# Optimization experiments

Measured on AMD Instinct MI355X. Metric: run time of the kernel, lower is better.

The kernel has to match this reference:

```python
import jax, jax.numpy as jnp
import numpy as np

# --- Mamba2Enc config (matches init_kwargs + mamba_ssm Mamba2 defaults) ---
D_IN = 1024
D_MODEL = 512
N_CLASSES = 2
NLAYERS = 2
D_STATE = 64
D_CONV = 4
EXPAND = 2
HEADDIM = 64
D_INNER = EXPAND * D_MODEL            # 1024
NHEADS = D_INNER // HEADDIM           # 16
CONV_DIM = D_INNER + 2 * D_STATE      # 1152 (ngroups=1)
D_IN_PROJ = 2 * D_INNER + 2 * D_STATE + NHEADS  # 2192
EPS = 1e-5


def setup_inputs() -> dict:
    key = jax.random.key(0)
    ks = jax.random.split(key, 10)
    def w(k, shape, sc=0.02):
        return jax.random.normal(k, shape, jnp.float32) * sc
    x = jax.random.normal(ks[0], (4, 4096, D_IN), jnp.float32)
    # fc1
    W1 = w(ks[1], (D_MODEL, D_IN))
    b1 = jnp.zeros((D_MODEL,), jnp.float32)
    # per-layer params stacked on leading NLAYERS axis
    ln_w = jnp.ones((NLAYERS, D_MODEL), jnp.float32)
    ln_b = jnp.zeros((NLAYERS, D_MODEL), jnp.float32)
    W_in = w(ks[2], (NLAYERS, D_IN_PROJ, D_MODEL))
    conv_w = w(ks[3], (NLAYERS, CONV_DIM, D_CONV), 0.1)
    conv_b = jnp.zeros((NLAYERS, CONV_DIM), jnp.float32)
    # dt_bias so that softplus(dt_bias) ~ [0.001, 0.1] (mamba init range)
    dt_bias = jax.random.uniform(ks[4], (NLAYERS, NHEADS), jnp.float32, -6.0, -2.3)
    A_log = jnp.log(jnp.tile(jnp.arange(1, NHEADS + 1, dtype=jnp.float32), (NLAYERS, 1)))
    Dskip = jnp.ones((NLAYERS, NHEADS), jnp.float32)
    norm_w = jnp.ones((NLAYERS, D_INNER), jnp.float32)
    W_out = w(ks[5], (NLAYERS, D_MODEL, D_INNER))
    # classifier
    Wc = w(ks[6], (N_CLASSES, D_MODEL))
    bc = jnp.zeros((N_CLASSES,), jnp.float32)
    return dict(x=x, W1=W1, b1=b1, ln_w=ln_w, ln_b=ln_b, W_in=W_in,
                conv_w=conv_w, conv_b=conv_b, dt_bias=dt_bias, A_log=A_log,
                Dskip=Dskip, norm_w=norm_w, W_out=W_out, Wc=Wc, bc=bc)


def _layernorm(h, w, b):
    mu = jnp.mean(h, axis=-1, keepdims=True)
    var = jnp.mean(jnp.square(h - mu), axis=-1, keepdims=True)
    return (h - mu) * jax.lax.rsqrt(var + EPS) * w + b


def _silu(x):
    return x * jax.nn.sigmoid(x)


def _mamba2(x, W_in, conv_w, conv_b, dt_bias, A_log, Dskip, norm_w, W_out):
    b, l, _ = x.shape
    zxbcdt = jnp.einsum('bld,ed->ble', x, W_in)  # (b, l, D_IN_PROJ)
    z = zxbcdt[..., :D_INNER]
    xBC = zxbcdt[..., D_INNER:D_INNER + CONV_DIM]
    dt = jax.nn.softplus(zxbcdt[..., -NHEADS:] + dt_bias)  # (b, l, h)
    # causal depthwise conv1d (kernel D_CONV) + silu
    xp = jnp.pad(xBC, ((0, 0), (D_CONV - 1, 0), (0, 0)))
    xBC = sum(xp[:, k:k + l, :] * conv_w[:, k] for k in range(D_CONV)) + conv_b
    xBC = _silu(xBC)
    xh = xBC[..., :D_INNER].reshape(b, l, NHEADS, HEADDIM)
    B = xBC[..., D_INNER:D_INNER + D_STATE]   # (b, l, n) ngroups=1
    C = xBC[..., D_INNER + D_STATE:]          # (b, l, n)
    A = -jnp.exp(A_log)                       # (h,)
    dA = jnp.exp(dt * A)                      # (b, l, h)
    dtx = dt[..., None] * xh                  # (b, l, h, p)

    def step(hstate, inp):
        dA_t, dtx_t, B_t, C_t = inp  # (b,h), (b,h,p), (b,n), (b,n)
        hstate = hstate * dA_t[:, :, None, None] + dtx_t[:, :, None, :] * B_t[:, None, :, None]
        y = jnp.einsum('bn,bhnp->bhp', C_t, hstate)
        return hstate, y

    init = jnp.zeros((b, NHEADS, D_STATE, HEADDIM), x.dtype)
    xs = (dA.transpose(1, 0, 2), dtx.transpose(1, 0, 2, 3),
          B.transpose(1, 0, 2), C.transpose(1, 0, 2))
    _, ys = jax.lax.scan(step, init, xs)      # ys: (l, b, h, p)
    y = ys.transpose(1, 0, 2, 3) + Dskip[None, None, :, None] * xh
    y = y.reshape(b, l, D_INNER)
    # RMSNormGated (norm_before_gate=False): rmsnorm(y * silu(z)) * weight
    y = y * _silu(z)
    y = y * jax.lax.rsqrt(jnp.mean(jnp.square(y), axis=-1, keepdims=True) + EPS) * norm_w
    return jnp.einsum('ble,de->bld', y, W_out)


def reference(x, W1, b1, ln_w, ln_b, W_in, conv_w, conv_b, dt_bias, A_log,
              Dskip, norm_w, W_out, Wc, bc):
    # fc1: Linear + GELU (dropout is identity at eval)
    h = jax.nn.gelu(jnp.einsum('bli,di->bld', x, W1) + b1, approximate=False)
    for i in range(NLAYERS):
        h = h + _mamba2(_layernorm(h, ln_w[i], ln_b[i]), W_in[i], conv_w[i],
                        conv_b[i], dt_bias[i], A_log[i], Dskip[i], norm_w[i], W_out[i])
    return jnp.einsum('bld,cd->blc', h, Wc) + bc
```

## Files before the change

kernel.cpp:

```cpp
#include <hip/hip_runtime.h>
#include <hip/hip_bf16.h>
#include <math.h>

#define BATCH 4
#define SEQ 4096
#define ROWS 16384
#define DIN 1024
#define DMODEL 512
#define DINNER 1024
#define DSTATE 64
#define NH 16
#define HD 64
#define CONVDIM 1152
#define DPROJ 2192
#define NPAD 2304
#define QC 64
#define NCH 64
#define LD 72

typedef __attribute__((ext_vector_type(8))) __bf16 bf16x8;
typedef __attribute__((ext_vector_type(4))) __bf16 bf16x4;
typedef __attribute__((ext_vector_type(4))) float f32x4;

__device__ __forceinline__ float siluf(float x){ return x / (1.f + __expf(-x)); }
__device__ __forceinline__ float geluf(float x){ return 0.5f*x*(1.f + erff(x*0.70710678118654752440f)); }

__device__ __forceinline__ bf16x8 scale8(bf16x8 v, float s){
  bf16x8 r;
  #pragma unroll
  for (int e = 0; e < 8; e++) r[e] = (__bf16)((float)v[e]*s);
  return r;
}

__device__ __forceinline__ void gl_lds16(const void* g, void* l){
  __builtin_amdgcn_global_load_lds((const __attribute__((address_space(1))) void*)g,
                                   (__attribute__((address_space(3))) void*)l, 16, 0, 0);
}

__device__ __forceinline__ bf16x8 cvt8(const float* sp){
  const float4* p = (const float4*)sp;
  float4 a = p[0], b = p[1];
  bf16x8 o;
  o[0]=(__bf16)a.x; o[1]=(__bf16)a.y; o[2]=(__bf16)a.z; o[3]=(__bf16)a.w;
  o[4]=(__bf16)b.x; o[5]=(__bf16)b.y; o[6]=(__bf16)b.z; o[7]=(__bf16)b.w;
  return o;
}

__global__ void cast_bf16_kernel(const float* __restrict__ src, __bf16* __restrict__ dst, long n8){
  long i = (long)blockIdx.x*blockDim.x + threadIdx.x;
  long stride = (long)gridDim.x*blockDim.x;
  for (; i < n8; i += stride) *(bf16x8*)(dst + i*8) = cvt8(src + i*8);
}

#define W1G   (DMODEL*DIN/8)
#define WOG   (2*DMODEL*DINNER/8)
#define WIG   (2L*NPAD*(DMODEL/8))
__global__ void prep_weights(const float* __restrict__ W1, const float* __restrict__ W_out,
                             const float* __restrict__ W_in, __bf16* __restrict__ W1b,
                             __bf16* __restrict__ Woutb, __bf16* __restrict__ Winb){
  long total = W1G + WOG + WIG;
  long i = (long)blockIdx.x*blockDim.x + threadIdx.x;
  long stride = (long)gridDim.x*blockDim.x;
  for (; i < total; i += stride){
    if (i < W1G){
      *(bf16x8*)(W1b + i*8) = cvt8(W1 + i*8);
    } else if (i < W1G + WOG){
      long j = i - W1G;
      *(bf16x8*)(Woutb + j*8) = cvt8(W_out + j*8);
    } else {
      long j = i - W1G - WOG;
      int k8 = (int)(j % (DMODEL/8));
      int n  = (int)((j / (DMODEL/8)) % NPAD);
      int l  = (int)(j / ((long)(DMODEL/8)*NPAD));
      bf16x8 o;
      if (n < DPROJ){
        o = cvt8(W_in + ((long)l*DPROJ + n)*DMODEL + k8*8);
      } else {
        #pragma unroll
        for (int e = 0; e < 8; e++) o[e] = (__bf16)0.f;
      }
      *(bf16x8*)(Winb + ((long)l*NPAD + n)*DMODEL + k8*8) = o;
    }
  }
}

template<typename OutT, int EPI, int BM, int BN>
__global__ __launch_bounds__(256) void gemm_bt(const __bf16* __restrict__ A, const __bf16* __restrict__ Bm,
                                               OutT* __restrict__ C, const float* __restrict__ bias,
                                               int K, int Nc, int nbm){
  constexpr int MI = BM/32, NI = BN/32;
  constexpr int CHA = BM/64;
  constexpr int CHT = (BM+BN)/64;
  __shared__ __align__(16) __bf16 As[3][BM*32];
  __shared__ __align__(16) __bf16 Bs[3][BN*32];
  int nwg = gridDim.x;
  int cpx = nwg >> 3;
  int lin = blockIdx.x;
  int swz = (lin & 7)*cpx + (lin >> 3);
  int bm = swz % nbm, bn = swz / nbm;
  int tid = threadIdx.x;
  int lane = tid & 63, wid = tid >> 6;
  int wm = (wid >> 1)*(BM/2), wn = (wid & 1)*(BN/2);
  int lr = lane & 15, kb = lane >> 4;
  f32x4 acc[MI][NI] = {};
  const char* Ab = (const char*)A + (size_t)bm*BM*(size_t)(K*2);
  const char* Bb = (const char*)Bm + (size_t)bn*BN*(size_t)(K*2);
  int nkk = K >> 5;

  auto STAGE = [&](int kk, int buf){
    #pragma unroll
    for (int it = 0; it < CHT; it++){
      int cbase = it*4096 + wid*1024;
      int off = cbase + lane*16;
      int row = off >> 6, cb = off & 63;
      if (it < CHA) gl_lds16(Ab + (size_t)row*(K*2) + kk*64 + cb, (char*)(&As[buf][0]) + cbase);
      else          gl_lds16(Bb + (size_t)(row - BM)*(K*2) + kk*64 + cb, (char*)(&Bs[buf][0]) + (cbase - BM*64));
    }
  };

  STAGE(0, 0);
  if (nkk > 1) STAGE(1, 1);
  for (int kk = 0; kk < nkk; kk++){
    int cur = kk % 3;
    if (kk + 2 < nkk){
      STAGE(kk + 2, (kk + 2) % 3);
      asm volatile("s_waitcnt vmcnt(%0)" :: "n"(2*CHT) : "memory");
    } else if (kk + 1 < nkk){
      asm volatile("s_waitcnt vmcnt(%0)" :: "n"(CHT) : "memory");
    } else {
      asm volatile("s_waitcnt vmcnt(0)" ::: "memory");
    }
    __builtin_amdgcn_sched_barrier(0);
    __builtin_amdgcn_s_barrier();
    __builtin_amdgcn_sched_barrier(0);
    const __bf16* Asb = &As[cur][0];
    const __bf16* Bsb = &Bs[cur][0];
    bf16x8 af[MI], bfr[NI];
    #pragma unroll
    for (int mi = 0; mi < MI; mi++) af[mi] = *(const bf16x8*)(Asb + (wm + mi*16 + lr)*32 + kb*8);
    #pragma unroll
    for (int ni = 0; ni < NI; ni++) bfr[ni] = *(const bf16x8*)(Bsb + (wn + ni*16 + lr)*32 + kb*8);
    #pragma unroll
    for (int mi = 0; mi < MI; mi++)
      #pragma unroll
      for (int ni = 0; ni < NI; ni++)
        acc[mi][ni] = __builtin_amdgcn_mfma_f32_16x16x32_bf16(af[mi], bfr[ni], acc[mi][ni], 0, 0, 0);
    __builtin_amdgcn_s_barrier();
    __builtin_amdgcn_sched_barrier(0);
  }
  #pragma unroll
  for (int mi = 0; mi < MI; mi++){
    #pragma unroll
    for (int ni = 0; ni < NI; ni++){
      int r0 = bm*BM + wm + mi*16 + (lane >> 4)*4;
      int c  = bn*BN + wn + ni*16 + lr;
      if (c < Nc){
        OutT* Cp = C + (size_t)r0*Nc + c;
        #pragma unroll
        for (int j = 0; j < 4; j++){
          float v = acc[mi][ni][j];
          if (EPI == 1){ float u = v + bias[c]; v = geluf(u); }
          if (EPI == 2){ v += (float)Cp[(size_t)j*Nc]; }
          Cp[(size_t)j*Nc] = (OutT)v;
        }
      }
    }
  }
}

__global__ __launch_bounds__(256) void ln_kernel(const __bf16* __restrict__ h, const float* __restrict__ w,
                                                 const float* __restrict__ b, __bf16* __restrict__ out){
  int row = blockIdx.x*4 + (threadIdx.x >> 6);
  int lane = threadIdx.x & 63;
  const __bf16* hr = h + (size_t)row*DMODEL + lane*8;
  bf16x8 a = *(const bf16x8*)hr;
  float v[8];
  #pragma unroll
  for (int i = 0; i < 8; i++) v[i] = (float)a[i];
  float s = 0.f;
  #pragma unroll
  for (int i = 0; i < 8; i++) s += v[i];
  #pragma unroll
  for (int o = 32; o; o >>= 1) s += __shfl_xor(s, o, 64);
  float mu = s*(1.f/512.f);
  float q = 0.f;
  #pragma unroll
  for (int i = 0; i < 8; i++){ float d = v[i]-mu; q += d*d; }
  #pragma unroll
  for (int o = 32; o; o >>= 1) q += __shfl_xor(q, o, 64);
  float rs = rsqrtf(q*(1.f/512.f) + 1e-5f);
  const float* wp = w + lane*8; const float* bp = b + lane*8;
  bf16x8 o8;
  #pragma unroll
  for (int i = 0; i < 8; i++) o8[i] = (__bf16)((v[i]-mu)*rs*wp[i] + bp[i]);
  *(bf16x8*)(out + (size_t)row*DMODEL + lane*8) = o8;
}

__global__ __launch_bounds__(256) void convdt_kernel(const __bf16* __restrict__ zx, const float* __restrict__ cw,
                                                     const float* __restrict__ cb, const float* __restrict__ dt_bias,
                                                     __bf16* __restrict__ BCc, float* __restrict__ dtT){
  long idx = (long)blockIdx.x*256 + threadIdx.x;
  long bt = idx / 144;
  int j = (int)(idx - bt*144);
  if (bt >= ROWS) return;
  int t = (int)(bt & (SEQ-1));
  int b = (int)(bt >> 12);
  if (j < 128){
    int ch = DINNER + j;
    const __bf16* src = zx + (size_t)bt*DPROJ + 2048 + j;
    float acc = cb[ch] + (float)src[0]*cw[ch*4+3];
    if (t >= 1) acc += (float)src[-1L*DPROJ]*cw[ch*4+2];
    if (t >= 2) acc += (float)src[-2L*DPROJ]*cw[ch*4+1];
    if (t >= 3) acc += (float)src[-3L*DPROJ]*cw[ch*4+0];
    BCc[(size_t)bt*128 + j] = (__bf16)siluf(acc);
  } else {
    int hh = j - 128;
    float v = (float)zx[(size_t)bt*DPROJ + (DPROJ-NH) + hh] + dt_bias[hh];
    float sp = (v > 20.f) ? v : log1pf(__expf(v));
    dtT[((size_t)b*NH + hh)*SEQ + t] = sp;
  }
}

__global__ __launch_bounds__(128) void ssd_state(const __bf16* __restrict__ zx, const __bf16* __restrict__ BCc,
                                                 const float* __restrict__ dtT, const float* __restrict__ A_log,
                                                 const float* __restrict__ cw, const float* __restrict__ cb,
                                                 __bf16* __restrict__ Schunk, float* __restrict__ Pbuf,
                                                 __bf16* __restrict__ xhT){
  __shared__ __align__(16) __bf16 Bt_all[2][64*LD];
  __shared__ __align__(16) __bf16 Xt_all[2][64*LD];
  int widx = threadIdx.x >> 6, lane = threadIdx.x & 63;
  int c = blockIdx.x*2 + widx, h = blockIdx.y, b = blockIdx.z;
  __bf16* Bt = Bt_all[widx];
  __bf16* Xt = Xt_all[widx];
  int lr = lane & 15, kb = lane >> 4, hi4 = lane >> 4;
  long t0 = (long)c*QC;
  size_t bt0 = (size_t)b*SEQ + t0;
  int bh = b*NH + h;
  float Ac = -expf(A_log[h]);
  float dtv = dtT[(size_t)bh*SEQ + t0 + lane];
  float cum = dtv*Ac;
  #pragma unroll
  for (int off = 1; off < 64; off <<= 1){ float v = __shfl_up(cum, off, 64); if (lane >= off) cum += v; }
  float cumQ = __shfl(cum, 63, 64);
  float w = __expf(cumQ - cum) * dtv;
  {
    const __bf16* bp = BCc + bt0*128 + lane;
    for (int tb = 0; tb < 8; tb++){
      bf16x8 buf;
      #pragma unroll
      for (int u = 0; u < 8; u++){
        int t = tb*8 + u;
        float bv = (float)bp[(size_t)t*128];
        buf[u] = (__bf16)(bv * __shfl(w, t, 64));
      }
      *(bf16x8*)&Bt[lane*LD + tb*8] = buf;
    }
  }
  {
    int ch = h*HD + lane;
    float w0 = cw[ch*4], w1 = cw[ch*4+1], w2 = cw[ch*4+2], w3 = cw[ch*4+3], cbv = cb[ch];
    const __bf16* xp = zx + bt0*DPROJ + (DINNER + ch);
    float x1 = (t0 >= 1) ? (float)xp[-1L*DPROJ] : 0.f;
    float x2 = (t0 >= 2) ? (float)xp[-2L*DPROJ] : 0.f;
    float x3 = (t0 >= 3) ? (float)xp[-3L*DPROJ] : 0.f;
    __bf16* xo = xhT + ((size_t)bh*NCH + c)*4096 + lane*64;
    for (int tb = 0; tb < 8; tb++){
      bf16x8 buf;
      #pragma unroll
      for (int u = 0; u < 8; u++){
        int t = tb*8 + u;
        float x0 = (float)xp[(size_t)t*DPROJ];
        float xv = siluf(cbv + w3*x0 + w2*x1 + w1*x2 + w0*x3);
        x3 = x2; x2 = x1; x1 = x0;
        buf[u] = (__bf16)xv;
      }
      *(bf16x8*)&Xt[lane*LD + tb*8] = buf;
      *(bf16x8*)(xo + tb*8) = buf;
    }
  }
  f32x4 acc[4][4] = {};
  #pragma unroll
  for (int kk = 0; kk < 2; kk++){
    bf16x8 af[4], bfr[4];
    #pragma unroll
    for (int mi = 0; mi < 4; mi++) af[mi]  = *(bf16x8*)&Bt[(mi*16+lr)*LD + kk*32 + kb*8];
    #pragma unroll
    for (int ni = 0; ni < 4; ni++) bfr[ni] = *(bf16x8*)&Xt[(ni*16+lr)*LD + kk*32 + kb*8];
    #pragma unroll
    for (int mi = 0; mi < 4; mi++)
      #pragma unroll
      for (int ni = 0; ni < 4; ni++)
        acc[mi][ni] = __builtin_amdgcn_mfma_f32_16x16x32_bf16(af[mi], bfr[ni], acc[mi][ni], 0, 0, 0);
  }
  __bf16* Sp = Schunk + ((size_t)bh*NCH + c)*4096;
  #pragma unroll
  for (int mi = 0; mi < 4; mi++)
    #pragma unroll
    for (int ni = 0; ni < 4; ni++){
      int n0 = mi*16 + hi4*4;
      int p  = ni*16 + lr;
      bf16x4 v;
      #pragma unroll
      for (int r = 0; r < 4; r++) v[r] = (__bf16)acc[mi][ni][r];
      *(bf16x4*)&Sp[p*64 + n0] = v;
    }
  if (lane == 0) Pbuf[bh*NCH + c] = __expf(cumQ);
}

__global__ __launch_bounds__(64) void ssd_comb(__bf16* __restrict__ Schunk, const float* __restrict__ Pbuf){
  int bh = blockIdx.x >> 4;
  int eb = blockIdx.x & 15;
  int e = eb*256 + threadIdx.x*4;
  __bf16* base = Schunk + (size_t)bh*NCH*4096 + e;
  float T0 = 0.f, T1 = 0.f, T2 = 0.f, T3 = 0.f;
  for (int c = 0; c < NCH; c++){
    float P = Pbuf[bh*NCH + c];
    bf16x4* p = (bf16x4*)(base + (size_t)c*4096);
    bf16x4 s = *p;
    bf16x4 o; o[0] = (__bf16)T0; o[1] = (__bf16)T1; o[2] = (__bf16)T2; o[3] = (__bf16)T3;
    *p = o;
    T0 = T0*P + (float)s[0]; T1 = T1*P + (float)s[1];
    T2 = T2*P + (float)s[2]; T3 = T3*P + (float)s[3];
  }
}

__global__ __launch_bounds__(256) void ssd_y(const __bf16* __restrict__ BCc, const float* __restrict__ dtT,
                                             const float* __restrict__ A_log, const float* __restrict__ Dskip,
                                             const __bf16* __restrict__ xhT, const __bf16* __restrict__ Spre,
                                             __bf16* __restrict__ yout){
  __shared__ __align__(16) __bf16 Gs_all[4][64*LD];
  __shared__ float cum_all[4][64], dt_all[4][64];
  int widx = threadIdx.x >> 6, lane = threadIdx.x & 63;
  int c = blockIdx.x*4 + widx, h = blockIdx.y, b = blockIdx.z;
  __bf16* Gs = Gs_all[widx];
  float* cum_s = cum_all[widx];
  float* dt_s = dt_all[widx];
  int lr = lane & 15, kb = lane >> 4, hi4 = lane >> 4;
  long t0 = (long)c*QC;
  size_t bt0 = (size_t)b*SEQ + t0;
  int bh = b*NH + h;
  float Ac = -expf(A_log[h]);
  float Dk = Dskip[h];
  float dtv = dtT[(size_t)bh*SEQ + t0 + lane];
  float cum = dtv*Ac;
  #pragma unroll
  for (int off = 1; off < 64; off <<= 1){ float v = __shfl_up(cum, off, 64); if (lane >= off) cum += v; }
  cum_s[lane] = cum; dt_s[lane] = dtv;
  bf16x8 cf[4][2];
  #pragma unroll
  for (int ni = 0; ni < 4; ni++)
    #pragma unroll
    for (int kk = 0; kk < 2; kk++)
      cf[ni][kk] = *(const bf16x8*)&BCc[(bt0 + ni*16 + lr)*128 + 64 + kk*32 + kb*8];
  f32x4 g[4][4] = {};
  #pragma unroll
  for (int kk = 0; kk < 2; kk++){
    bf16x8 bfj[4];
    #pragma unroll
    for (int mi = 0; mi < 4; mi++) bfj[mi] = *(const bf16x8*)&BCc[(bt0 + mi*16 + lr)*128 + kk*32 + kb*8];
    #pragma unroll
    for (int mi = 0; mi < 4; mi++)
      #pragma unroll
      for (int ni = 0; ni < 4; ni++)
        g[mi][ni] = __builtin_amdgcn_mfma_f32_16x16x32_bf16(bfj[mi], cf[ni][kk], g[mi][ni], 0, 0, 0);
  }
  float cumi[4];
  #pragma unroll
  for (int ni = 0; ni < 4; ni++) cumi[ni] = cum_s[ni*16 + lr];
  #pragma unroll
  for (int mi = 0; mi < 4; mi++){
    #pragma unroll
    for (int r = 0; r < 4; r++){
      int j = mi*16 + hi4*4 + r;
      float cj = cum_s[j], dj = dt_s[j];
      #pragma unroll
      for (int ni = 0; ni < 4; ni++){
        int i = ni*16 + lr;
        float v = g[mi][ni][r];
        if (i > j)       v = v * __expf(cumi[ni] - cj) * dj;
        else if (i == j) v = v*dj + Dk;
        else             v = 0.f;
        g[mi][ni][r] = v;
      }
    }
  }
  #pragma unroll
  for (int mi = 0; mi < 4; mi++)
    #pragma unroll
    for (int ni = 0; ni < 4; ni++){
      int j0 = mi*16 + hi4*4;
      int i  = ni*16 + lr;
      bf16x4 v;
      #pragma unroll
      for (int r = 0; r < 4; r++) v[r] = (__bf16)g[mi][ni][r];
      *(bf16x4*)&Gs[i*LD + j0] = v;
    }
  const __bf16* Xp = xhT + ((size_t)bh*NCH + c)*4096;
  f32x4 y4[4][4] = {};
  #pragma unroll
  for (int kk = 0; kk < 2; kk++){
    bf16x8 af2[4], bf2[4];
    #pragma unroll
    for (int mi = 0; mi < 4; mi++) af2[mi] = *(const bf16x8*)&Xp[(mi*16+lr)*64 + kk*32 + kb*8];
    #pragma unroll
    for (int ni = 0; ni < 4; ni++) bf2[ni] = *(bf16x8*)&Gs[(ni*16+lr)*LD + kk*32 + kb*8];
    #pragma unroll
    for (int mi = 0; mi < 4; mi++)
      #pragma unroll
      for (int ni = 0; ni < 4; ni++)
        y4[mi][ni] = __builtin_amdgcn_mfma_f32_16x16x32_bf16(af2[mi], bf2[ni], y4[mi][ni], 0, 0, 0);
  }
  {
    const __bf16* Sp = Spre + ((size_t)bh*NCH + c)*4096;
    float ei[4];
    #pragma unroll
    for (int ni = 0; ni < 4; ni++) ei[ni] = __expf(cumi[ni]);
    #pragma unroll
    for (int kk = 0; kk < 2; kk++){
      bf16x8 as1[4];
      #pragma unroll
      for (int mi = 0; mi < 4; mi++) as1[mi] = *(const bf16x8*)&Sp[(mi*16+lr)*64 + kk*32 + kb*8];
      #pragma unroll
      for (int ni = 0; ni < 4; ni++){
        bf16x8 cs = scale8(cf[ni][kk], ei[ni]);
        #pragma unroll
        for (int mi = 0; mi < 4; mi++)
          y4[mi][ni] = __builtin_amdgcn_mfma_f32_16x16x32_bf16(as1[mi], cs, y4[mi][ni], 0, 0, 0);
      }
    }
  }
  #pragma unroll
  for (int mi = 0; mi < 4; mi++)
    #pragma unroll
    for (int ni = 0; ni < 4; ni++){
      int p0 = mi*16 + hi4*4;
      int i  = ni*16 + lr;
      bf16x4 v;
      #pragma unroll
      for (int r = 0; r < 4; r++) v[r] = (__bf16)y4[mi][ni][r];
      *(bf16x4*)&yout[(bt0 + i)*DINNER + h*HD + p0] = v;
    }
}

__global__ __launch_bounds__(256) void gate_rms(__bf16* __restrict__ y, const __bf16* __restrict__ zx,
                                                const float* __restrict__ nw){
  int row = blockIdx.x*4 + (threadIdx.x >> 6);
  int lane = threadIdx.x & 63;
  __bf16* yr = y + (size_t)row*DINNER + lane*16;
  const __bf16* zr = zx + (size_t)row*DPROJ + lane*16;
  bf16x8 y0 = *(const bf16x8*)yr, y1 = *(const bf16x8*)(yr+8);
  bf16x8 z0 = *(const bf16x8*)zr, z1 = *(const bf16x8*)(zr+8);
  float v[16]; float ss = 0.f;
  #pragma unroll
  for (int i = 0; i < 8; i++){ float z = (float)z0[i]; float tv = (float)y0[i]*siluf(z); v[i] = tv; ss += tv*tv; }
  #pragma unroll
  for (int i = 0; i < 8; i++){ float z = (float)z1[i]; float tv = (float)y1[i]*siluf(z); v[8+i] = tv; ss += tv*tv; }
  #pragma unroll
  for (int o = 32; o; o >>= 1) ss += __shfl_xor(ss, o, 64);
  float rs = rsqrtf(ss*(1.f/1024.f) + 1e-5f);
  const float* np = nw + lane*16;
  bf16x8 o0, o1;
  #pragma unroll
  for (int i = 0; i < 8; i++){ o0[i] = (__bf16)(v[i]*rs*np[i]); o1[i] = (__bf16)(v[8+i]*rs*np[8+i]); }
  *(bf16x8*)yr = o0; *(bf16x8*)(yr+8) = o1;
}

__global__ __launch_bounds__(256) void cls_kernel(const __bf16* __restrict__ h, const float* __restrict__ Wc,
                                                  const float* __restrict__ bc, float* __restrict__ out){
  int row = blockIdx.x*4 + (threadIdx.x >> 6);
  int lane = threadIdx.x & 63;
  const __bf16* hr = h + (size_t)row*DMODEL + lane*8;
  bf16x8 a = *(const bf16x8*)hr;
  float hv[8];
  #pragma unroll
  for (int i = 0; i < 8; i++) hv[i] = (float)a[i];
  const float* w0 = Wc + lane*8;
  const float* w1 = Wc + DMODEL + lane*8;
  float s0 = 0.f, s1 = 0.f;
  #pragma unroll
  for (int i = 0; i < 8; i++){ s0 += hv[i]*w0[i]; s1 += hv[i]*w1[i]; }
  #pragma unroll
  for (int o = 32; o; o >>= 1){ s0 += __shfl_xor(s0, o, 64); s1 += __shfl_xor(s1, o, 64); }
  if (lane == 0){ out[(size_t)row*2] = s0 + bc[0]; out[(size_t)row*2 + 1] = s1 + bc[1]; }
}

extern "C" void kernel_launch(void* const* d_in, const int* in_sizes, int n_in,
                              void* d_out, int out_size, void* d_ws, size_t ws_size,
                              hipStream_t stream){
  const float* x       = (const float*)d_in[0];
  const float* W1      = (const float*)d_in[1];
  const float* b1      = (const float*)d_in[2];
  const float* ln_w    = (const float*)d_in[3];
  const float* ln_b    = (const float*)d_in[4];
  const float* W_in    = (const float*)d_in[5];
  const float* conv_w  = (const float*)d_in[6];
  const float* conv_b  = (const float*)d_in[7];
  const float* dt_bias = (const float*)d_in[8];
  const float* A_log   = (const float*)d_in[9];
  const float* Dskip   = (const float*)d_in[10];
  const float* norm_w  = (const float*)d_in[11];
  const float* W_out   = (const float*)d_in[12];
  const float* Wc      = (const float*)d_in[13];
  const float* bc      = (const float*)d_in[14];
  float* out = (float*)d_out;
  char* ws = (char*)d_ws;

  size_t off = 0;
  auto alloc = [&](size_t bytes){ void* p = ws + off; off += (bytes + 255) & ~(size_t)255; return p; };
  char*   regionA = (char*) alloc((size_t)ROWS*DIN*2);
  __bf16* W1b     = (__bf16*)alloc((size_t)DMODEL*DIN*2);
  __bf16* Winb    = (__bf16*)alloc(2L*NPAD*DMODEL*2);
  __bf16* Woutb   = (__bf16*)alloc(2L*DMODEL*DINNER*2);
  __bf16* h       = (__bf16*)alloc((size_t)ROWS*DMODEL*2);
  __bf16* zx      = (__bf16*)alloc((size_t)ROWS*DPROJ*2);
  __bf16* BCc     = (__bf16*)alloc((size_t)ROWS*128*2);
  float*  dtT     = (float*) alloc((size_t)ROWS*NH*4);
  __bf16* ybuf    = (__bf16*)alloc((size_t)ROWS*DINNER*2);
  __bf16* xhT     = (__bf16*)alloc((size_t)ROWS*DINNER*2);
  float*  Pbuf    = (float*) alloc(64L*NCH*4);
  if (off > ws_size) return;

  __bf16* x_bf   = (__bf16*)regionA;
  __bf16* hnb    = (__bf16*)regionA;
  __bf16* Schunk = (__bf16*)regionA;

  cast_bf16_kernel<<<2048, 256, 0, stream>>>(x, x_bf, (long)ROWS*DIN/8);
  prep_weights<<<1024, 256, 0, stream>>>(W1, W_out, W_in, W1b, Woutb, Winb);

  gemm_bt<__bf16,1,64,128><<<(ROWS/64)*(DMODEL/128), 256, 0, stream>>>(x_bf, W1b, h, b1, DIN, DMODEL, ROWS/64);

  for (int l = 0; l < 2; l++){
    ln_kernel<<<ROWS/4, 256, 0, stream>>>(h, ln_w + l*DMODEL, ln_b + l*DMODEL, hnb);
    gemm_bt<__bf16,0,128,128><<<(ROWS/128)*(NPAD/128), 256, 0, stream>>>(hnb, Winb + (size_t)l*NPAD*DMODEL,
                                                                          zx, nullptr, DMODEL, DPROJ, ROWS/128);
    convdt_kernel<<<(ROWS*144 + 255)/256, 256, 0, stream>>>(zx, conv_w + l*CONVDIM*4, conv_b + l*CONVDIM,
                                                            dt_bias + l*NH, BCc, dtT);
    {
      dim3 gs(NCH/2, NH, BATCH);
      ssd_state<<<gs, 128, 0, stream>>>(zx, BCc, dtT, A_log + l*NH,
                                        conv_w + l*CONVDIM*4, conv_b + l*CONVDIM, Schunk, Pbuf, xhT);
      ssd_comb<<<64*16, 64, 0, stream>>>(Schunk, Pbuf);
      dim3 gy(NCH/4, NH, BATCH);
      ssd_y<<<gy, 256, 0, stream>>>(BCc, dtT, A_log + l*NH, Dskip + l*NH, xhT, Schunk, ybuf);
    }
    gate_rms<<<ROWS/4, 256, 0, stream>>>(ybuf, zx, norm_w + l*DINNER);
    gemm_bt<__bf16,2,64,128><<<(ROWS/64)*(DMODEL/128), 256, 0, stream>>>(ybuf, Woutb + (size_t)l*DMODEL*DINNER,
                                                                          h, nullptr, DINNER, DMODEL, ROWS/64);
  }

  cls_kernel<<<ROWS/4, 256, 0, stream>>>(h, Wc, bc, out);
}
```

Measured before the change: 518.7 us.

## Vectorize conv/dt kernel and drop XCD block swizzle in GEMMs

```diff
diff --git a/kernel.cpp b/kernel.cpp
--- a/kernel.cpp
+++ b/kernel.cpp
@@ -87,17 +87,13 @@
 template<typename OutT, int EPI, int BM, int BN>
 __global__ __launch_bounds__(256) void gemm_bt(const __bf16* __restrict__ A, const __bf16* __restrict__ Bm,
                                                OutT* __restrict__ C, const float* __restrict__ bias,
-                                               int K, int Nc, int nbm){
+                                               int K, int Nc){
   constexpr int MI = BM/32, NI = BN/32;
   constexpr int CHA = BM/64;
   constexpr int CHT = (BM+BN)/64;
   __shared__ __align__(16) __bf16 As[3][BM*32];
   __shared__ __align__(16) __bf16 Bs[3][BN*32];
-  int nwg = gridDim.x;
-  int cpx = nwg >> 3;
-  int lin = blockIdx.x;
-  int swz = (lin & 7)*cpx + (lin >> 3);
-  int bm = swz % nbm, bn = swz / nbm;
+  int bm = blockIdx.x, bn = blockIdx.y;
   int tid = threadIdx.x;
   int lane = tid & 63, wid = tid >> 6;
   int wm = (wid >> 1)*(BM/2), wn = (wid & 1)*(BN/2);
@@ -200,21 +196,32 @@
                                                      const float* __restrict__ cb, const float* __restrict__ dt_bias,
                                                      __bf16* __restrict__ BCc, float* __restrict__ dtT){
   long idx = (long)blockIdx.x*256 + threadIdx.x;
-  long bt = idx / 144;
-  int j = (int)(idx - bt*144);
+  long bt = idx >> 5;
+  int j = (int)(idx & 31);
   if (bt >= ROWS) return;
   int t = (int)(bt & (SEQ-1));
   int b = (int)(bt >> 12);
-  if (j < 128){
-    int ch = DINNER + j;
-    const __bf16* src = zx + (size_t)bt*DPROJ + 2048 + j;
-    float acc = cb[ch] + (float)src[0]*cw[ch*4+3];
-    if (t >= 1) acc += (float)src[-1L*DPROJ]*cw[ch*4+2];
-    if (t >= 2) acc += (float)src[-2L*DPROJ]*cw[ch*4+1];
-    if (t >= 3) acc += (float)src[-3L*DPROJ]*cw[ch*4+0];
-    BCc[(size_t)bt*128 + j] = (__bf16)siluf(acc);
+  if (j < 16){
+    int c0 = j*8;
+    const __bf16* src = zx + (size_t)bt*DPROJ + 2048 + c0;
+    bf16x8 v0 = *(const bf16x8*)src;
+    bf16x8 v1, v2, v3;
+    #pragma unroll
+    for (int e = 0; e < 8; e++){ v1[e] = (__bf16)0.f; v2[e] = (__bf16)0.f; v3[e] = (__bf16)0.f; }
+    if (t >= 1) v1 = *(const bf16x8*)(src - 1L*DPROJ);
+    if (t >= 2) v2 = *(const bf16x8*)(src - 2L*DPROJ);
+    if (t >= 3) v3 = *(const bf16x8*)(src - 3L*DPROJ);
+    bf16x8 o;
+    #pragma unroll
+    for (int e = 0; e < 8; e++){
+      int ch = DINNER + c0 + e;
+      float acc = cb[ch] + (float)v0[e]*cw[ch*4+3] + (float)v1[e]*cw[ch*4+2]
+                + (float)v2[e]*cw[ch*4+1] + (float)v3[e]*cw[ch*4+0];
+      o[e] = (__bf16)siluf(acc);
+    }
+    *(bf16x8*)(BCc + (size_t)bt*128 + c0) = o;
   } else {
-    int hh = j - 128;
+    int hh = j - 16;
     float v = (float)zx[(size_t)bt*DPROJ + (DPROJ-NH) + hh] + dt_bias[hh];
     float sp = (v > 20.f) ? v : log1pf(__expf(v));
     dtT[((size_t)b*NH + hh)*SEQ + t] = sp;
@@ -527,14 +534,19 @@
   cast_bf16_kernel<<<2048, 256, 0, stream>>>(x, x_bf, (long)ROWS*DIN/8);
   prep_weights<<<1024, 256, 0, stream>>>(W1, W_out, W_in, W1b, Woutb, Winb);
 
-  gemm_bt<__bf16,1,64,128><<<(ROWS/64)*(DMODEL/128), 256, 0, stream>>>(x_bf, W1b, h, b1, DIN, DMODEL, ROWS/64);
+  {
+    dim3 g(ROWS/64, DMODEL/128);
+    gemm_bt<__bf16,1,64,128><<<g, 256, 0, stream>>>(x_bf, W1b, h, b1, DIN, DMODEL);
+  }
 
   for (int l = 0; l < 2; l++){
     ln_kernel<<<ROWS/4, 256, 0, stream>>>(h, ln_w + l*DMODEL, ln_b + l*DMODEL, hnb);
-    gemm_bt<__bf16,0,128,128><<<(ROWS/128)*(NPAD/128), 256, 0, stream>>>(hnb, Winb + (size_t)l*NPAD*DMODEL,
-                                                                          zx, nullptr, DMODEL, DPROJ, ROWS/128);
-    convdt_kernel<<<(ROWS*144 + 255)/256, 256, 0, stream>>>(zx, conv_w + l*CONVDIM*4, conv_b + l*CONVDIM,
-                                                            dt_bias + l*NH, BCc, dtT);
+    {
+      dim3 g(ROWS/128, NPAD/128);
+      gemm_bt<__bf16,0,128,128><<<g, 256, 0, stream>>>(hnb, Winb + (size_t)l*NPAD*DMODEL, zx, nullptr, DMODEL, DPROJ);
+    }
+    convdt_kernel<<<(ROWS*32)/256, 256, 0, stream>>>(zx, conv_w + l*CONVDIM*4, conv_b + l*CONVDIM,
+                                                     dt_bias + l*NH, BCc, dtT);
     {
       dim3 gs(NCH/2, NH, BATCH);
       ssd_state<<<gs, 128, 0, stream>>>(zx, BCc, dtT, A_log + l*NH,
@@ -544,8 +556,10 @@
       ssd_y<<<gy, 256, 0, stream>>>(BCc, dtT, A_log + l*NH, Dskip + l*NH, xhT, Schunk, ybuf);
     }
     gate_rms<<<ROWS/4, 256, 0, stream>>>(ybuf, zx, norm_w + l*DINNER);
-    gemm_bt<__bf16,2,64,128><<<(ROWS/64)*(DMODEL/128), 256, 0, stream>>>(ybuf, Woutb + (size_t)l*DMODEL*DINNER,
-                                                                          h, nullptr, DINNER, DMODEL, ROWS/64);
+    {
+      dim3 g(ROWS/64, DMODEL/128);
+      gemm_bt<__bf16,2,64,128><<<g, 256, 0, stream>>>(ybuf, Woutb + (size_t)l*DMODEL*DINNER, h, nullptr, DINNER, DMODEL);
+    }
   }
 
   cls_kernel<<<ROWS/4, 256, 0, stream>>>(h, Wc, bc, out);
```

Measured after the change: 471.4 us (median of 2 runs). -9.1%, faster.
